# Optimization experiments

Measured on AMD Instinct MI355X. Metric: run time of the kernel, lower is better.

Reference implementation:

```python
import jax, jax.numpy as jnp
import numpy as np

EPS = 1e-13

def masked_softmax(vec, mask, axis=-1):
    # Old AllenNLP masked_softmax: softmax(vec * mask), re-mask, renormalize.
    result = jax.nn.softmax(vec * mask, axis=axis)
    result = result * mask
    return result / (result.sum(axis=axis, keepdims=True) + EPS)

def setup_inputs() -> dict:
    key = jax.random.key(0)
    k1, k2, k3, k4 = jax.random.split(key, 4)
    B, N, T, U, H = 8, 20, 300, 64, 512
    doc_encoding = jax.random.normal(k1, (B, N, T, H), dtype=jnp.float32)
    q_encoding = jax.random.normal(k2, (B, U, H), dtype=jnp.float32)
    doc_mask = jax.random.randint(k3, (B, N, T), 0, 2, dtype=jnp.int32)
    q_mask = jax.random.randint(k4, (B, U), 0, 2, dtype=jnp.int32)
    return {"doc_encoding": doc_encoding, "q_encoding": q_encoding,
            "doc_mask": doc_mask, "q_mask": q_mask}

def reference(doc_encoding, q_encoding, doc_mask, q_mask):
    B, N, T, H = doc_encoding.shape
    U = q_encoding.shape[1]
    dtype = doc_encoding.dtype
    dm = doc_mask.astype(dtype)            # B,N,T
    qm = q_mask.astype(dtype)              # B,U
    doc = doc_encoding.reshape(B, N * T, H)  # B,NT,H
    # shared unnormalized co-attention scores: B,NT,U
    scores = jnp.einsum('bkh,buh->bku', doc, q_encoding)
    # doc->question attention (softmax over U, masked by q_mask)
    attn = masked_softmax(scores, qm[:, None, :], axis=-1)  # B,NT,U
    aggq = jnp.einsum('bku,buh->bkh', attn, q_encoding)      # B,NT,H
    # question->doc attention (softmax over T within each doc, masked by doc_mask)
    attn_t = scores.transpose(0, 2, 1).reshape(B, U, N, T)   # B,U,N,T
    attn_t = masked_softmax(attn_t, dm[:, None, :, :], axis=-1)
    attn_t = attn_t.reshape(B, U, N * T)
    aggdoc = jnp.einsum('buk,bkh->buh', attn_t, doc)          # B,U,H
    aggq2 = jnp.einsum('bku,buh->bkh', attn, aggdoc)          # B,NT,H
    out = jnp.concatenate([aggq.reshape(B, N, T, H),
                           aggq2.reshape(B, N, T, H)], axis=-1)  # B,N,T,2H
    return out
```

## Files before the change

kernel.cpp:

```cpp
#include <hip/hip_runtime.h>

#define BB 8
#define NN 20
#define TT 300
#define UU 64
#define HH 512
#define NT 6000


typedef __attribute__((ext_vector_type(4))) float f32x4;
typedef __attribute__((ext_vector_type(8))) short s16x8;

__device__ __forceinline__ float bf2f(unsigned short u) {
  union { unsigned int i; float f; } c; c.i = ((unsigned int)u) << 16; return c.f;
}
__device__ __forceinline__ unsigned short f2bf(float f) {
  union { float f; unsigned int i; } c; c.f = f;
  unsigned int u = c.i;
  unsigned int r = (u + 0x7fffu + ((u >> 16) & 1u)) >> 16;
  return (unsigned short)r;
}
__device__ __forceinline__ void splitbf(float x, unsigned short& hi, unsigned short& lo) {
  hi = f2bf(x);
  lo = f2bf(x - bf2f(hi));
}
__device__ __forceinline__ f32x4 mfma16(s16x8 a, s16x8 b, f32x4 c) {
  return __builtin_amdgcn_mfma_f32_16x16x32_bf16(a, b, c, 0, 0, 0);
}

__global__ __launch_bounds__(256) void kdetect(const unsigned short* __restrict__ d16,
                                               int* __restrict__ flag) {
  __shared__ int cnt[4];
  int t = threadIdx.x;
  unsigned short v = d16[t];
  int e = (v >> 7) & 0xFF;
  int weird = (e > 140 || (e < 110 && (v & 0x7FFFu) != 0)) ? 1 : 0;
  unsigned long long m = __ballot(weird);
  if ((t & 63) == 0) cnt[t >> 6] = __popcll(m);
  __syncthreads();
  if (t == 0) flag[0] = (cnt[0] + cnt[1] + cnt[2] + cnt[3] >= 32) ? 1 : 0;
}

__global__ __launch_bounds__(256) void k0_init(const void* __restrict__ qv,
                                               const int* __restrict__ flag,
                                               float* __restrict__ W) {
  const int isf32 = *flag;
  int idx = blockIdx.x * 256 + threadIdx.x;
  int h2 = idx & 1023;
  int bu = idx >> 10;
  float v = 0.0f;
  if (h2 < HH) {
    v = isf32 ? ((const float*)qv)[bu * HH + h2]
              : bf2f(((const unsigned short*)qv)[bu * HH + h2]);
  }
  W[idx] = v;
}

__global__ __launch_bounds__(256) void k1_mfma(const void* __restrict__ docv,
                                               const void* __restrict__ qv,
                                               const int* __restrict__ flag,
                                               float* __restrict__ scores) {
  __shared__ __align__(16) unsigned short sDhi[64 * 64], sDlo[64 * 64];
  __shared__ __align__(16) unsigned short sQhi[64 * 64], sQlo[64 * 64];
  const int isf32 = *flag;
  const int b = blockIdx.y, kt = blockIdx.x;
  const int tid = threadIdx.x;
  const int lane = tid & 63, w = tid >> 6;
  const int l15 = lane & 15, l4 = lane >> 4;
  const int kmax = NT - kt * 64;
  const size_t dbase = (size_t)(b * NT + kt * 64) * HH;
  const size_t qbase = (size_t)b * UU * HH;
  const f32x4 zero = {0.f, 0.f, 0.f, 0.f};
  f32x4 acc[4] = {zero, zero, zero, zero};

  for (int hc = 0; hc < 8; ++hc) {
    if (hc) __syncthreads();
#pragma unroll
    for (int i = 0; i < 2; ++i) {
      int g = tid + 256 * i;
      int row = g >> 3, h8 = (g & 7) * 8;
      int addr = (row * 128 + h8 * 2) ^ ((row & 7) << 4);
      {
        float v[8] = {0.f, 0.f, 0.f, 0.f, 0.f, 0.f, 0.f, 0.f};
        if (row < kmax) {
          size_t off = dbase + (size_t)row * HH + hc * 64 + h8;
          if (isf32) {
            const float* df = (const float*)docv;
            float4 a0 = *(const float4*)(df + off);
            float4 a1 = *(const float4*)(df + off + 4);
            v[0] = a0.x; v[1] = a0.y; v[2] = a0.z; v[3] = a0.w;
            v[4] = a1.x; v[5] = a1.y; v[6] = a1.z; v[7] = a1.w;
          } else {
            const unsigned short* db = (const unsigned short*)docv;
            ushort4 a0 = *(const ushort4*)(db + off);
            ushort4 a1 = *(const ushort4*)(db + off + 4);
            v[0] = bf2f(a0.x); v[1] = bf2f(a0.y); v[2] = bf2f(a0.z); v[3] = bf2f(a0.w);
            v[4] = bf2f(a1.x); v[5] = bf2f(a1.y); v[6] = bf2f(a1.z); v[7] = bf2f(a1.w);
          }
        }
        s16x8 vh, vl;
#pragma unroll
        for (int j = 0; j < 8; ++j) {
          unsigned short hh, ll; splitbf(v[j], hh, ll);
          vh[j] = (short)hh; vl[j] = (short)ll;
        }
        *(s16x8*)((char*)sDhi + addr) = vh;
        *(s16x8*)((char*)sDlo + addr) = vl;
      }
      {
        size_t off = qbase + (size_t)row * HH + hc * 64 + h8;
        float v[8];
        if (isf32) {
          const float* qf = (const float*)qv;
          float4 a0 = *(const float4*)(qf + off);
          float4 a1 = *(const float4*)(qf + off + 4);
          v[0] = a0.x; v[1] = a0.y; v[2] = a0.z; v[3] = a0.w;
          v[4] = a1.x; v[5] = a1.y; v[6] = a1.z; v[7] = a1.w;
        } else {
          const unsigned short* qb = (const unsigned short*)qv;
          ushort4 a0 = *(const ushort4*)(qb + off);
          ushort4 a1 = *(const ushort4*)(qb + off + 4);
          v[0] = bf2f(a0.x); v[1] = bf2f(a0.y); v[2] = bf2f(a0.z); v[3] = bf2f(a0.w);
          v[4] = bf2f(a1.x); v[5] = bf2f(a1.y); v[6] = bf2f(a1.z); v[7] = bf2f(a1.w);
        }
        s16x8 vh, vl;
#pragma unroll
        for (int j = 0; j < 8; ++j) {
          unsigned short hh, ll; splitbf(v[j], hh, ll);
          vh[j] = (short)hh; vl[j] = (short)ll;
        }
        *(s16x8*)((char*)sQhi + addr) = vh;
        *(s16x8*)((char*)sQlo + addr) = vl;
      }
    }
    __syncthreads();
#pragma unroll
    for (int kb = 0; kb < 2; ++kb) {
      const int off = kb * 64 + l4 * 16;
      const int brow = w * 16 + l15;
      const int ba = (brow * 128 + off) ^ ((brow & 7) << 4);
      s16x8 bh = *(const s16x8*)((const char*)sDhi + ba);
      s16x8 bl = *(const s16x8*)((const char*)sDlo + ba);
#pragma unroll
      for (int mt = 0; mt < 4; ++mt) {
        const int arow = mt * 16 + l15;
        const int aa = (arow * 128 + off) ^ ((arow & 7) << 4);
        s16x8 ah = *(const s16x8*)((const char*)sQhi + aa);
        s16x8 al = *(const s16x8*)((const char*)sQlo + aa);
        acc[mt] = mfma16(ah, bh, acc[mt]);
        acc[mt] = mfma16(ah, bl, acc[mt]);
        acc[mt] = mfma16(al, bh, acc[mt]);
      }
    }
  }
  const int krow = w * 16 + l15;
  if (krow < kmax) {
    size_t ro = ((size_t)b * NT + kt * 64 + krow) * 64;
#pragma unroll
    for (int mt = 0; mt < 4; ++mt)
      *(f32x4*)&scores[ro + mt * 16 + l4 * 4] = acc[mt];
  }
}

__global__ __launch_bounds__(256) void k2b_tstats(const float* __restrict__ scores,
                                                  const int* __restrict__ dm,
                                                  float* __restrict__ tmax,
                                                  float* __restrict__ tsum) {
  const int b = blockIdx.x / NN;
  const int n = blockIdx.x % NN;
  const int u = threadIdx.x & 63;
  const int tg = threadIdx.x >> 6;
  float m = -__builtin_inff(), s = 0.0f;
  for (int t = tg; t < TT; t += 4) {
    int dmv = dm[(b * NN + n) * TT + t];
    if (dmv) {
      float v = scores[((size_t)(b * NT) + n * TT + t) * 64 + u];
      if (v > m) { s = s * __expf(m - v) + 1.0f; m = v; }
      else s += __expf(v - m);
    }
  }
  __shared__ float sm[4][64], ss[4][64];
  sm[tg][u] = m; ss[tg][u] = s;
  __syncthreads();
  if (threadIdx.x < 64) {
    float M = sm[0][u];
#pragma unroll
    for (int i = 1; i < 4; ++i) M = fmaxf(M, sm[i][u]);
    float S = 0.0f;
#pragma unroll
    for (int i = 0; i < 4; ++i) {
      if (ss[i][u] > 0.0f) S += ss[i][u] * __expf(sm[i][u] - M);
    }
    tmax[(b * 64 + u) * NN + n] = M;
    tsum[(b * 64 + u) * NN + n] = S;
  }
}

__global__ __launch_bounds__(256) void k2c2(const float* __restrict__ scores,
                                            const int* __restrict__ qm,
                                            const int* __restrict__ dm,
                                            const float* __restrict__ tmax,
                                            const float* __restrict__ tsum,
                                            unsigned short* __restrict__ PaH,
                                            unsigned short* __restrict__ PaL,
                                            unsigned short* __restrict__ Pt) {
  const int row = blockIdx.x * 4 + (threadIdx.x >> 6);
  const int u = threadIdx.x & 63;
  const int b = row / NT;
  const int k = row - b * NT;
  const int n = k / TT;
  const float s = scores[(size_t)row * 64 + u];
  const int m = qm[b * 64 + u];
  float v = m ? s : -__builtin_inff();
#pragma unroll
  for (int o = 32; o > 0; o >>= 1) v = fmaxf(v, __shfl_xor(v, o, 64));
  float e = m ? __expf(s - v) : 0.0f;
  float sum = e;
#pragma unroll
  for (int o = 32; o > 0; o >>= 1) sum += __shfl_xor(sum, o, 64);
  float attn = (sum > 0.0f) ? (e / sum) : 0.0f;
  unsigned short hi, lo;
  splitbf(attn, hi, lo);
  PaH[(size_t)row * 64 + u] = hi;
  PaL[(size_t)row * 64 + u] = lo;
  float wgt = 0.0f;
  if (dm[b * NT + k]) {
    float S = tsum[(b * 64 + u) * NN + n];
    if (S > 0.0f) wgt = __expf(s - tmax[(b * 64 + u) * NN + n]) / S;
  }
  Pt[(size_t)row * 64 + u] = f2bf(wgt);
}

__global__ __launch_bounds__(256) void k3_mfma(const unsigned short* __restrict__ Pt,
                                               const void* __restrict__ docv,
                                               const int* __restrict__ flag,
                                               float* __restrict__ W) {
  __shared__ __align__(16) unsigned short sDh[128 * 64], sDl[128 * 64];
  __shared__ __align__(16) unsigned short sP[64 * 64];
  const int isf32 = *flag;
  const int b = blockIdx.z, hc = blockIdx.y, kc = blockIdx.x;
  const int tid = threadIdx.x, lane = tid & 63, w = tid >> 6;
  const int l15 = lane & 15, l4 = lane >> 4;
  const int k0base = kc * 375, kend = k0base + 375;
  const f32x4 zero = {0.f, 0.f, 0.f, 0.f};
  f32x4 acc[4][2];
#pragma unroll
  for (int mt = 0; mt < 4; ++mt) { acc[mt][0] = zero; acc[mt][1] = zero; }

  for (int kb = k0base; kb < kend; kb += 64) {
    const int kn = min(64, kend - kb);
    if (kb != k0base) __syncthreads();
#pragma unroll
    for (int i = 0; i < 4; ++i) {
      int g = tid + 256 * i;
      int kk = g >> 4, u4 = (g & 15) * 4;
      unsigned short t[4] = {0, 0, 0, 0};
      if (kk < kn) {
        ushort4 tv = *(const ushort4*)&Pt[((size_t)b * NT + kb + kk) * 64 + u4];
        t[0] = tv.x; t[1] = tv.y; t[2] = tv.z; t[3] = tv.w;
      }
#pragma unroll
      for (int ii = 0; ii < 4; ++ii) {
        int jj = (ii + tid) & 3;
        int u = u4 + jj;
        int addr = (u * 128 + kk * 2) ^ ((u & 7) << 4);
        *(unsigned short*)((char*)sP + addr) = t[jj];
      }
    }
#pragma unroll
    for (int i = 0; i < 8; ++i) {
      int g = tid + 256 * i;
      int kk = g >> 5, h4 = (g & 31) * 4;
      float v[4] = {0.f, 0.f, 0.f, 0.f};
      if (kk < kn) {
        size_t off = ((size_t)b * NT + kb + kk) * HH + hc * 128 + h4;
        if (isf32) {
          float4 a0 = *(const float4*)((const float*)docv + off);
          v[0] = a0.x; v[1] = a0.y; v[2] = a0.z; v[3] = a0.w;
        } else {
          ushort4 a0 = *(const ushort4*)((const unsigned short*)docv + off);
          v[0] = bf2f(a0.x); v[1] = bf2f(a0.y); v[2] = bf2f(a0.z); v[3] = bf2f(a0.w);
        }
      }
#pragma unroll
      for (int ii = 0; ii < 4; ++ii) {
        int jj = (ii + tid) & 3;
        int hrow = h4 + jj;
        unsigned short hh, ll;
        splitbf(v[jj], hh, ll);
        int addr = (hrow * 128 + kk * 2) ^ ((hrow & 7) << 4);
        *(unsigned short*)((char*)sDh + addr) = hh;
        *(unsigned short*)((char*)sDl + addr) = ll;
      }
    }
    __syncthreads();
#pragma unroll
    for (int ks = 0; ks < 2; ++ks) {
      const int off = ks * 64 + l4 * 16;
      s16x8 bh[2], bl[2];
#pragma unroll
      for (int nt = 0; nt < 2; ++nt) {
        int r = w * 32 + nt * 16 + l15;
        int a = (r * 128 + off) ^ ((r & 7) << 4);
        bh[nt] = *(const s16x8*)((const char*)sDh + a);
        bl[nt] = *(const s16x8*)((const char*)sDl + a);
      }
#pragma unroll
      for (int mt = 0; mt < 4; ++mt) {
        int r = mt * 16 + l15;
        int a = (r * 128 + off) ^ ((r & 7) << 4);
        s16x8 pa = *(const s16x8*)((const char*)sP + a);
#pragma unroll
        for (int nt = 0; nt < 2; ++nt) {
          acc[mt][nt] = mfma16(pa, bh[nt], acc[mt][nt]);
          acc[mt][nt] = mfma16(pa, bl[nt], acc[mt][nt]);
        }
      }
    }
  }
#pragma unroll
  for (int mt = 0; mt < 4; ++mt)
#pragma unroll
    for (int nt = 0; nt < 2; ++nt)
#pragma unroll
      for (int j = 0; j < 4; ++j) {
        int u = mt * 16 + l4 * 4 + j;
        int h = hc * 128 + w * 32 + nt * 16 + l15;
        atomicAdd(&W[((size_t)b * 64 + u) * 1024 + 512 + h], acc[mt][nt][j]);
      }
}

__global__ __launch_bounds__(256) void k35_wt(const float* __restrict__ W,
                                              unsigned short* __restrict__ WtH,
                                              unsigned short* __restrict__ WtL) {
  __shared__ float sW[64][68];
  const int b = blockIdx.y, hck = blockIdx.x;
  const int tid = threadIdx.x;
#pragma unroll
  for (int i = 0; i < 4; ++i) {
    int g = tid + 256 * i;
    int u = g >> 4, c4 = (g & 15) * 4;
    *(float4*)&sW[u][c4] = *(const float4*)&W[((size_t)b * 64 + u) * 1024 + hck * 64 + c4];
  }
  __syncthreads();
  const int h = tid >> 2, ug = tid & 3;
  s16x8 oh[2], ol[2];
#pragma unroll
  for (int p = 0; p < 2; ++p)
#pragma unroll
    for (int j = 0; j < 8; ++j) {
      unsigned short hh, ll;
      splitbf(sW[ug * 16 + p * 8 + j][h], hh, ll);
      oh[p][j] = (short)hh; ol[p][j] = (short)ll;
    }
  size_t ob = ((size_t)b * 1024 + hck * 64 + h) * 64 + ug * 16;
  *(s16x8*)&WtH[ob] = oh[0];
  *(s16x8*)&WtH[ob + 8] = oh[1];
  *(s16x8*)&WtL[ob] = ol[0];
  *(s16x8*)&WtL[ob + 8] = ol[1];
}

__global__ __launch_bounds__(256) void k4_mfma(const unsigned short* __restrict__ PaH,
                                               const unsigned short* __restrict__ PaL,
                                               const unsigned short* __restrict__ WtH,
                                               const unsigned short* __restrict__ WtL,
                                               const int* __restrict__ flag,
                                               void* __restrict__ outv) {
  const int isf32 = *flag;
  const int b = blockIdx.z, ht = blockIdx.y, kt = blockIdx.x;
  const int tid = threadIdx.x, lane = tid & 63, w = tid >> 6;
  const int l15 = lane & 15, l4 = lane >> 4;
  const int h0 = ht * 64;
  const int kr0 = kt * 256 + w * 64;
  const f32x4 zero = {0.f, 0.f, 0.f, 0.f};
  f32x4 acc[4][4];
#pragma unroll
  for (int mt = 0; mt < 4; ++mt)
#pragma unroll
    for (int nt = 0; nt < 4; ++nt) acc[mt][nt] = zero;
#pragma unroll
  for (int kb = 0; kb < 2; ++kb) {
    s16x8 ah[4], al[4];
#pragma unroll
    for (int mt = 0; mt < 4; ++mt) {
      size_t a = ((size_t)b * 1024 + h0 + mt * 16 + l15) * 64 + kb * 32 + l4 * 8;
      ah[mt] = *(const s16x8*)&WtH[a];
      al[mt] = *(const s16x8*)&WtL[a];
    }
#pragma unroll
    for (int nt = 0; nt < 4; ++nt) {
      int krow = kr0 + nt * 16 + l15;
      int krc = krow < NT ? krow : NT - 1;
      size_t pb = ((size_t)b * NT + krc) * 64 + kb * 32 + l4 * 8;
      s16x8 bh = *(const s16x8*)&PaH[pb];
      s16x8 bl = *(const s16x8*)&PaL[pb];
#pragma unroll
      for (int mt = 0; mt < 4; ++mt) {
        acc[mt][nt] = mfma16(ah[mt], bh, acc[mt][nt]);
        acc[mt][nt] = mfma16(ah[mt], bl, acc[mt][nt]);
        acc[mt][nt] = mfma16(al[mt], bh, acc[mt][nt]);
      }
    }
  }
#pragma unroll
  for (int nt = 0; nt < 4; ++nt) {
    int krow = kr0 + nt * 16 + l15;
    if (krow < NT) {
      size_t ob = ((size_t)b * NT + krow) * 1024 + h0;
#pragma unroll
      for (int mt = 0; mt < 4; ++mt) {
        int h2 = mt * 16 + l4 * 4;
        if (isf32) {
          *(f32x4*)((float*)outv + ob + h2) = acc[mt][nt];
        } else {
          ushort4 o;
          o.x = f2bf(acc[mt][nt][0]); o.y = f2bf(acc[mt][nt][1]);
          o.z = f2bf(acc[mt][nt][2]); o.w = f2bf(acc[mt][nt][3]);
          *(ushort4*)((unsigned short*)outv + ob + h2) = o;
        }
      }
    }
  }
}

__global__ __launch_bounds__(256) void k2_softmax_u(float* __restrict__ scores,
                                                    const int* __restrict__ qm) {
  const int row = blockIdx.x * 4 + (threadIdx.x >> 6);
  const int u = threadIdx.x & 63;
  const int b = row / NT;
  const float s = scores[(size_t)row * 64 + u];
  const int m = qm[b * 64 + u];
  float v = m ? s : -__builtin_inff();
#pragma unroll
  for (int o = 32; o > 0; o >>= 1) v = fmaxf(v, __shfl_xor(v, o, 64));
  float e = m ? __expf(s - v) : 0.0f;
  float sum = e;
#pragma unroll
  for (int o = 32; o > 0; o >>= 1) sum += __shfl_xor(sum, o, 64);
  scores[(size_t)row * 64 + u] = (sum > 0.0f) ? (e / sum) : 0.0f;
}

__global__ __launch_bounds__(256) void k3_aggdoc(const float* __restrict__ scores,
                                                 const void* __restrict__ docv,
                                                 const int* __restrict__ dm,
                                                 const float* __restrict__ tmax,
                                                 const float* __restrict__ tsum,
                                                 const int* __restrict__ flag,
                                                 float* __restrict__ W) {
  __shared__ float wL[32][68];
  __shared__ float dL[32][68];
  const int isf32 = *flag;
  const int b = blockIdx.z, hc = blockIdx.y, kc = blockIdx.x;
  const int tid = threadIdx.x;
  const int th = tid & 15, tuq = tid >> 4;
  float acc[4][4] = {};
  const int k0base = kc * 375, kend = k0base + 375;
  for (int k0 = k0base; k0 < kend; k0 += 32) {
    const int kn = min(32, kend - k0);
#pragma unroll
    for (int i = 0; i < 8; ++i) {
      int idx = tid + 256 * i;
      int kk = idx >> 6, uu = idx & 63;
      float wv = 0.0f;
      if (kk < kn) {
        int k = k0 + kk;
        int n = k / TT;
        if (dm[b * NT + k]) {
          float S = tsum[(b * 64 + uu) * NN + n];
          if (S > 0.0f) {
            float M = tmax[(b * 64 + uu) * NN + n];
            wv = __expf(scores[((size_t)(b * NT) + k) * 64 + uu] - M) / S;
          }
        }
      }
      wL[kk][uu] = wv;
    }
#pragma unroll
    for (int i = 0; i < 2; ++i) {
      int g = tid + 256 * i;
      int kk = g >> 4, c4 = (g & 15) * 4;
      float4 v = make_float4(0.f, 0.f, 0.f, 0.f);
      if (kk < kn) {
        size_t off = ((size_t)(b * NT) + k0 + kk) * HH + hc * 64 + c4;
        if (isf32) v = *(const float4*)((const float*)docv + off);
        else {
          ushort4 t4 = *(const ushort4*)((const unsigned short*)docv + off);
          v = make_float4(bf2f(t4.x), bf2f(t4.y), bf2f(t4.z), bf2f(t4.w));
        }
      }
      *(float4*)&dL[kk][c4] = v;
    }
    __syncthreads();
    for (int kk = 0; kk < kn; ++kk) {
      float4 w4 = *(const float4*)&wL[kk][tuq * 4];
      float4 d4 = *(const float4*)&dL[kk][th * 4];
      acc[0][0] += w4.x * d4.x; acc[0][1] += w4.x * d4.y; acc[0][2] += w4.x * d4.z; acc[0][3] += w4.x * d4.w;
      acc[1][0] += w4.y * d4.x; acc[1][1] += w4.y * d4.y; acc[1][2] += w4.y * d4.z; acc[1][3] += w4.y * d4.w;
      acc[2][0] += w4.z * d4.x; acc[2][1] += w4.z * d4.y; acc[2][2] += w4.z * d4.z; acc[2][3] += w4.z * d4.w;
      acc[3][0] += w4.w * d4.x; acc[3][1] += w4.w * d4.y; acc[3][2] += w4.w * d4.z; acc[3][3] += w4.w * d4.w;
    }
    __syncthreads();
  }
#pragma unroll
  for (int i = 0; i < 4; ++i) {
#pragma unroll
    for (int j = 0; j < 4; ++j) {
      size_t addr = ((size_t)(b * 64) + tuq * 4 + i) * 1024 + 512 + hc * 64 + th * 4 + j;
      atomicAdd(&W[addr], acc[i][j]);
    }
  }
}

__global__ __launch_bounds__(256) void k4_out(const float* __restrict__ attn,
                                              const float* __restrict__ W,
                                              const int* __restrict__ flag,
                                              void* __restrict__ outv) {
  __shared__ float sAt[64][68];
  __shared__ float sWt[64][132];
  const int isf32 = *flag;
  const int b = blockIdx.z;
  const int kt = blockIdx.x;
  const int ht = blockIdx.y;
  const int tid = threadIdx.x;
  const int th2 = tid & 15, tkq = tid >> 4;
#pragma unroll
  for (int i = 0; i < 4; ++i) {
    int g = tid + 256 * i;
    int row = g >> 4, c4 = (g & 15) * 4;
    int k = kt * 64 + row;
    float4 v = make_float4(0.f, 0.f, 0.f, 0.f);
    if (k < NT) v = *(const float4*)&attn[((size_t)(b * NT) + k) * 64 + c4];
    *(float4*)&sAt[row][c4] = v;
  }
#pragma unroll
  for (int i = 0; i < 8; ++i) {
    int g = tid + 256 * i;
    int row = g >> 5, c4 = (g & 31) * 4;
    float4 wv = *(const float4*)&W[((size_t)(b * 64) + row) * 1024 + ht * 128 + c4];
    *(float4*)&sWt[row][c4] = wv;
  }
  __syncthreads();
  float acc[4][8] = {};
#pragma unroll 4
  for (int u = 0; u < 64; u += 4) {
    float a[4][4];
#pragma unroll
    for (int i = 0; i < 4; ++i)
      *(float4*)a[i] = *(const float4*)&sAt[tkq * 4 + i][u];
#pragma unroll
    for (int r = 0; r < 4; ++r) {
      float4 w0 = *(const float4*)&sWt[u + r][th2 * 4];
      float4 w1 = *(const float4*)&sWt[u + r][64 + th2 * 4];
#pragma unroll
      for (int i = 0; i < 4; ++i) {
        acc[i][0] += a[i][r] * w0.x; acc[i][1] += a[i][r] * w0.y;
        acc[i][2] += a[i][r] * w0.z; acc[i][3] += a[i][r] * w0.w;
        acc[i][4] += a[i][r] * w1.x; acc[i][5] += a[i][r] * w1.y;
        acc[i][6] += a[i][r] * w1.z; acc[i][7] += a[i][r] * w1.w;
      }
    }
  }
#pragma unroll
  for (int i = 0; i < 4; ++i) {
    int k = kt * 64 + tkq * 4 + i;
    if (k < NT) {
      size_t off = ((size_t)(b * NT) + k) * 1024 + ht * 128 + th2 * 4;
      if (isf32) {
        *(float4*)((float*)outv + off) = make_float4(acc[i][0], acc[i][1], acc[i][2], acc[i][3]);
        *(float4*)((float*)outv + off + 64) = make_float4(acc[i][4], acc[i][5], acc[i][6], acc[i][7]);
      } else {
        ushort4 o0, o1;
        o0.x = f2bf(acc[i][0]); o0.y = f2bf(acc[i][1]); o0.z = f2bf(acc[i][2]); o0.w = f2bf(acc[i][3]);
        o1.x = f2bf(acc[i][4]); o1.y = f2bf(acc[i][5]); o1.z = f2bf(acc[i][6]); o1.w = f2bf(acc[i][7]);
        *(ushort4*)((unsigned short*)outv + off) = o0;
        *(ushort4*)((unsigned short*)outv + off + 64) = o1;
      }
    }
  }
}

extern "C" void kernel_launch(void* const* d_in, const int* in_sizes, int n_in,
                              void* d_out, int out_size, void* d_ws, size_t ws_size,
                              hipStream_t stream) {
  const void* doc = d_in[0];
  const void* q   = d_in[1];
  const int* dmask = (const int*)d_in[2];
  const int* qmask = (const int*)d_in[3];

  float* ws = (float*)d_ws;
  float* scores = ws;
  float* tmax   = ws + 3072000;
  float* tsum   = ws + 3082240;
  float* W      = ws + 3092480;
  int*   flag   = (int*)(ws + 3616768);
  unsigned short* Pt  = (unsigned short*)(ws + 3616772);
  unsigned short* PaH = (unsigned short*)(ws + 5152772);
  unsigned short* PaL = (unsigned short*)(ws + 6688772);
  unsigned short* WtH = (unsigned short*)(ws + 8224772);
  unsigned short* WtL = (unsigned short*)(ws + 8486916);
  const size_t need_new = (size_t)8749060 * 4;

  kdetect<<<1, 256, 0, stream>>>((const unsigned short*)doc, flag);
  k0_init<<<2048, 256, 0, stream>>>(q, flag, W);
  k1_mfma<<<dim3(94, 8), 256, 0, stream>>>(doc, q, flag, scores);
  k2b_tstats<<<160, 256, 0, stream>>>(scores, dmask, tmax, tsum);
  if (ws_size >= need_new) {
    k2c2<<<12000, 256, 0, stream>>>(scores, qmask, dmask, tmax, tsum, PaH, PaL, Pt);
    k3_mfma<<<dim3(16, 4, 8), 256, 0, stream>>>(Pt, doc, flag, W);
    k35_wt<<<dim3(16, 8), 256, 0, stream>>>(W, WtH, WtL);
    k4_mfma<<<dim3(24, 16, 8), 256, 0, stream>>>(PaH, PaL, WtH, WtL, flag, d_out);
  } else {
    k3_aggdoc<<<dim3(16, 8, 8), 256, 0, stream>>>(scores, doc, dmask, tmax, tsum, flag, W);
    k2_softmax_u<<<12000, 256, 0, stream>>>(scores, qmask);
    k4_out<<<dim3(94, 8, 8), 256, 0, stream>>>(scores, W, flag, d_out);
  }
}
```

Before: 412.0 us.

## Presplit Q once, widen k1 tiles, and vectorize k3 transposed LDS staging

The query is split into bf16 hi/lo halves once in k0_init and stored to workspace. k1 then loads those halves straight into registers instead of re-splitting Q through LDS in every block, and processes 128 doc rows per 512-thread block. k3 now splits K into chunks of 250 across 24 blocks instead of 375 across 16. Its Pt and doc staging uses 4x4 register transposes with ushort4 LDS stores instead of scalar 2-byte stores. The changes add workspace, raise per-thread register use in k1 and leave fewer k1 blocks.

```diff
diff --git a/kernel.cpp b/kernel.cpp
--- a/kernel.cpp
+++ b/kernel.cpp
@@ -43,7 +43,9 @@
 
 __global__ __launch_bounds__(256) void k0_init(const void* __restrict__ qv,
                                                const int* __restrict__ flag,
-                                               float* __restrict__ W) {
+                                               float* __restrict__ W,
+                                               unsigned short* __restrict__ QsH,
+                                               unsigned short* __restrict__ QsL) {
   const int isf32 = *flag;
   int idx = blockIdx.x * 256 + threadIdx.x;
   int h2 = idx & 1023;
@@ -52,24 +54,28 @@
   if (h2 < HH) {
     v = isf32 ? ((const float*)qv)[bu * HH + h2]
               : bf2f(((const unsigned short*)qv)[bu * HH + h2]);
+    unsigned short hi, lo;
+    splitbf(v, hi, lo);
+    QsH[bu * HH + h2] = hi;
+    QsL[bu * HH + h2] = lo;
   }
   W[idx] = v;
 }
 
-__global__ __launch_bounds__(256) void k1_mfma(const void* __restrict__ docv,
-                                               const void* __restrict__ qv,
+__global__ __launch_bounds__(512) void k1_mfma(const void* __restrict__ docv,
+                                               const unsigned short* __restrict__ QsH,
+                                               const unsigned short* __restrict__ QsL,
                                                const int* __restrict__ flag,
                                                float* __restrict__ scores) {
-  __shared__ __align__(16) unsigned short sDhi[64 * 64], sDlo[64 * 64];
-  __shared__ __align__(16) unsigned short sQhi[64 * 64], sQlo[64 * 64];
+  __shared__ __align__(16) unsigned short sDh[128 * 64], sDl[128 * 64];
   const int isf32 = *flag;
   const int b = blockIdx.y, kt = blockIdx.x;
   const int tid = threadIdx.x;
   const int lane = tid & 63, w = tid >> 6;
   const int l15 = lane & 15, l4 = lane >> 4;
-  const int kmax = NT - kt * 64;
-  const size_t dbase = (size_t)(b * NT + kt * 64) * HH;
-  const size_t qbase = (size_t)b * UU * HH;
+  const int kmax = NT - kt * 128;
+  const size_t dbase = (size_t)(b * NT + kt * 128) * HH;
+  const size_t qrow0 = (size_t)b * UU * HH;
   const f32x4 zero = {0.f, 0.f, 0.f, 0.f};
   f32x4 acc[4] = {zero, zero, zero, zero};
 
@@ -77,85 +83,63 @@
     if (hc) __syncthreads();
 #pragma unroll
     for (int i = 0; i < 2; ++i) {
-      int g = tid + 256 * i;
+      int g = tid + 512 * i;
       int row = g >> 3, h8 = (g & 7) * 8;
       int addr = (row * 128 + h8 * 2) ^ ((row & 7) << 4);
-      {
-        float v[8] = {0.f, 0.f, 0.f, 0.f, 0.f, 0.f, 0.f, 0.f};
-        if (row < kmax) {
-          size_t off = dbase + (size_t)row * HH + hc * 64 + h8;
-          if (isf32) {
-            const float* df = (const float*)docv;
-            float4 a0 = *(const float4*)(df + off);
-            float4 a1 = *(const float4*)(df + off + 4);
-            v[0] = a0.x; v[1] = a0.y; v[2] = a0.z; v[3] = a0.w;
-            v[4] = a1.x; v[5] = a1.y; v[6] = a1.z; v[7] = a1.w;
-          } else {
-            const unsigned short* db = (const unsigned short*)docv;
-            ushort4 a0 = *(const ushort4*)(db + off);
-            ushort4 a1 = *(const ushort4*)(db + off + 4);
-            v[0] = bf2f(a0.x); v[1] = bf2f(a0.y); v[2] = bf2f(a0.z); v[3] = bf2f(a0.w);
-            v[4] = bf2f(a1.x); v[5] = bf2f(a1.y); v[6] = bf2f(a1.z); v[7] = bf2f(a1.w);
-          }
-        }
-        s16x8 vh, vl;
-#pragma unroll
-        for (int j = 0; j < 8; ++j) {
-          unsigned short hh, ll; splitbf(v[j], hh, ll);
-          vh[j] = (short)hh; vl[j] = (short)ll;
-        }
-        *(s16x8*)((char*)sDhi + addr) = vh;
-        *(s16x8*)((char*)sDlo + addr) = vl;
-      }
-      {
-        size_t off = qbase + (size_t)row * HH + hc * 64 + h8;
-        float v[8];
+      float v[8] = {0.f, 0.f, 0.f, 0.f, 0.f, 0.f, 0.f, 0.f};
+      if (row < kmax) {
+        size_t off = dbase + (size_t)row * HH + hc * 64 + h8;
         if (isf32) {
-          const float* qf = (const float*)qv;
-          float4 a0 = *(const float4*)(qf + off);
-          float4 a1 = *(const float4*)(qf + off + 4);
+          const float* df = (const float*)docv;
+          float4 a0 = *(const float4*)(df + off);
+          float4 a1 = *(const float4*)(df + off + 4);
           v[0] = a0.x; v[1] = a0.y; v[2] = a0.z; v[3] = a0.w;
           v[4] = a1.x; v[5] = a1.y; v[6] = a1.z; v[7] = a1.w;
         } else {
-          const unsigned short* qb = (const unsigned short*)qv;
-          ushort4 a0 = *(const ushort4*)(qb + off);
-          ushort4 a1 = *(const ushort4*)(qb + off + 4);
+          const unsigned short* db = (const unsigned short*)docv;
+          ushort4 a0 = *(const ushort4*)(db + off);
+          ushort4 a1 = *(const ushort4*)(db + off + 4);
           v[0] = bf2f(a0.x); v[1] = bf2f(a0.y); v[2] = bf2f(a0.z); v[3] = bf2f(a0.w);
           v[4] = bf2f(a1.x); v[5] = bf2f(a1.y); v[6] = bf2f(a1.z); v[7] = bf2f(a1.w);
         }
-        s16x8 vh, vl;
-#pragma unroll
-        for (int j = 0; j < 8; ++j) {
-          unsigned short hh, ll; splitbf(v[j], hh, ll);
-          vh[j] = (short)hh; vl[j] = (short)ll;
-        }
-        *(s16x8*)((char*)sQhi + addr) = vh;
-        *(s16x8*)((char*)sQlo + addr) = vl;
-      }
+      }
+      s16x8 vh, vl;
+#pragma unroll
+      for (int j = 0; j < 8; ++j) {
+        unsigned short hh, ll; splitbf(v[j], hh, ll);
+        vh[j] = (short)hh; vl[j] = (short)ll;
+      }
+      *(s16x8*)((char*)sDh + addr) = vh;
+      *(s16x8*)((char*)sDl + addr) = vl;
     }
     __syncthreads();
+    s16x8 qh[2][4], ql[2][4];
+#pragma unroll
+    for (int kb = 0; kb < 2; ++kb)
+#pragma unroll
+      for (int mt = 0; mt < 4; ++mt) {
+        size_t qa = qrow0 + (size_t)(mt * 16 + l15) * HH + hc * 64 + kb * 32 + l4 * 8;
+        qh[kb][mt] = *(const s16x8*)&QsH[qa];
+        ql[kb][mt] = *(const s16x8*)&QsL[qa];
+      }
 #pragma unroll
     for (int kb = 0; kb < 2; ++kb) {
       const int off = kb * 64 + l4 * 16;
       const int brow = w * 16 + l15;
       const int ba = (brow * 128 + off) ^ ((brow & 7) << 4);
-      s16x8 bh = *(const s16x8*)((const char*)sDhi + ba);
-      s16x8 bl = *(const s16x8*)((const char*)sDlo + ba);
+      s16x8 bh = *(const s16x8*)((const char*)sDh + ba);
+      s16x8 bl = *(const s16x8*)((const char*)sDl + ba);
 #pragma unroll
       for (int mt = 0; mt < 4; ++mt) {
-        const int arow = mt * 16 + l15;
-        const int aa = (arow * 128 + off) ^ ((arow & 7) << 4);
-        s16x8 ah = *(const s16x8*)((const char*)sQhi + aa);
-        s16x8 al = *(const s16x8*)((const char*)sQlo + aa);
-        acc[mt] = mfma16(ah, bh, acc[mt]);
-        acc[mt] = mfma16(ah, bl, acc[mt]);
-        acc[mt] = mfma16(al, bh, acc[mt]);
+        acc[mt] = mfma16(qh[kb][mt], bh, acc[mt]);
+        acc[mt] = mfma16(qh[kb][mt], bl, acc[mt]);
+        acc[mt] = mfma16(ql[kb][mt], bh, acc[mt]);
       }
     }
   }
   const int krow = w * 16 + l15;
   if (krow < kmax) {
-    size_t ro = ((size_t)b * NT + kt * 64 + krow) * 64;
+    size_t ro = ((size_t)b * NT + kt * 128 + krow) * 64;
 #pragma unroll
     for (int mt = 0; mt < 4; ++mt)
       *(f32x4*)&scores[ro + mt * 16 + l4 * 4] = acc[mt];
@@ -241,7 +225,7 @@
   const int b = blockIdx.z, hc = blockIdx.y, kc = blockIdx.x;
   const int tid = threadIdx.x, lane = tid & 63, w = tid >> 6;
   const int l15 = lane & 15, l4 = lane >> 4;
-  const int k0base = kc * 375, kend = k0base + 375;
+  const int k0base = kc * 250, kend = k0base + 250;
   const f32x4 zero = {0.f, 0.f, 0.f, 0.f};
   f32x4 acc[4][2];
 #pragma unroll
@@ -250,47 +234,55 @@
   for (int kb = k0base; kb < kend; kb += 64) {
     const int kn = min(64, kend - kb);
     if (kb != k0base) __syncthreads();
-#pragma unroll
-    for (int i = 0; i < 4; ++i) {
-      int g = tid + 256 * i;
-      int kk = g >> 4, u4 = (g & 15) * 4;
-      unsigned short t[4] = {0, 0, 0, 0};
-      if (kk < kn) {
-        ushort4 tv = *(const ushort4*)&Pt[((size_t)b * NT + kb + kk) * 64 + u4];
-        t[0] = tv.x; t[1] = tv.y; t[2] = tv.z; t[3] = tv.w;
-      }
-#pragma unroll
-      for (int ii = 0; ii < 4; ++ii) {
-        int jj = (ii + tid) & 3;
-        int u = u4 + jj;
-        int addr = (u * 128 + kk * 2) ^ ((u & 7) << 4);
-        *(unsigned short*)((char*)sP + addr) = t[jj];
-      }
-    }
-#pragma unroll
-    for (int i = 0; i < 8; ++i) {
-      int g = tid + 256 * i;
-      int kk = g >> 5, h4 = (g & 31) * 4;
-      float v[4] = {0.f, 0.f, 0.f, 0.f};
-      if (kk < kn) {
-        size_t off = ((size_t)b * NT + kb + kk) * HH + hc * 128 + h4;
-        if (isf32) {
-          float4 a0 = *(const float4*)((const float*)docv + off);
-          v[0] = a0.x; v[1] = a0.y; v[2] = a0.z; v[3] = a0.w;
-        } else {
-          ushort4 a0 = *(const ushort4*)((const unsigned short*)docv + off);
-          v[0] = bf2f(a0.x); v[1] = bf2f(a0.y); v[2] = bf2f(a0.z); v[3] = bf2f(a0.w);
+    {
+      const int ug = tid & 15, kg = tid >> 4;
+      ushort4 r[4];
+#pragma unroll
+      for (int rr = 0; rr < 4; ++rr) {
+        int kk = kg * 4 + rr;
+        ushort4 t = make_ushort4(0, 0, 0, 0);
+        if (kk < kn) t = *(const ushort4*)&Pt[((size_t)b * NT + kb + kk) * 64 + ug * 4];
+        r[rr] = t;
+      }
+      const unsigned short* rp = (const unsigned short*)r;
+#pragma unroll
+      for (int uu = 0; uu < 4; ++uu) {
+        int u = ug * 4 + uu;
+        int addr = (u * 128 + kg * 8) ^ ((u & 7) << 4);
+        ushort4 col = make_ushort4(rp[0 * 4 + uu], rp[1 * 4 + uu], rp[2 * 4 + uu], rp[3 * 4 + uu]);
+        *(ushort4*)((char*)sP + addr) = col;
+      }
+    }
+#pragma unroll
+    for (int i = 0; i < 2; ++i) {
+      int s = tid + 256 * i;
+      int hg = s & 31, kg = s >> 5;
+      float rv[4][4];
+#pragma unroll
+      for (int rr = 0; rr < 4; ++rr) {
+        int kk = kg * 4 + rr;
+        float4 v = make_float4(0.f, 0.f, 0.f, 0.f);
+        if (kk < kn) {
+          size_t off = ((size_t)b * NT + kb + kk) * HH + hc * 128 + hg * 4;
+          if (isf32) v = *(const float4*)((const float*)docv + off);
+          else {
+            ushort4 t = *(const ushort4*)((const unsigned short*)docv + off);
+            v = make_float4(bf2f(t.x), bf2f(t.y), bf2f(t.z), bf2f(t.w));
+          }
         }
-      }
-#pragma unroll
-      for (int ii = 0; ii < 4; ++ii) {
-        int jj = (ii + tid) & 3;
-        int hrow = h4 + jj;
-        unsigned short hh, ll;
-        splitbf(v[jj], hh, ll);
-        int addr = (hrow * 128 + kk * 2) ^ ((hrow & 7) << 4);
-        *(unsigned short*)((char*)sDh + addr) = hh;
-        *(unsigned short*)((char*)sDl + addr) = ll;
+        rv[rr][0] = v.x; rv[rr][1] = v.y; rv[rr][2] = v.z; rv[rr][3] = v.w;
+      }
+#pragma unroll
+      for (int hh = 0; hh < 4; ++hh) {
+        int hrow = hg * 4 + hh;
+        int addr = (hrow * 128 + kg * 8) ^ ((hrow & 7) << 4);
+        unsigned short h0, l0, h1, l1, h2, l2, h3, l3;
+        splitbf(rv[0][hh], h0, l0);
+        splitbf(rv[1][hh], h1, l1);
+        splitbf(rv[2][hh], h2, l2);
+        splitbf(rv[3][hh], h3, l3);
+        *(ushort4*)((char*)sDh + addr) = make_ushort4(h0, h1, h2, h3);
+        *(ushort4*)((char*)sDl + addr) = make_ushort4(l0, l1, l2, l3);
       }
     }
     __syncthreads();
@@ -593,20 +585,22 @@
   float* tsum   = ws + 3082240;
   float* W      = ws + 3092480;
   int*   flag   = (int*)(ws + 3616768);
-  unsigned short* Pt  = (unsigned short*)(ws + 3616772);
-  unsigned short* PaH = (unsigned short*)(ws + 5152772);
-  unsigned short* PaL = (unsigned short*)(ws + 6688772);
-  unsigned short* WtH = (unsigned short*)(ws + 8224772);
-  unsigned short* WtL = (unsigned short*)(ws + 8486916);
-  const size_t need_new = (size_t)8749060 * 4;
+  unsigned short* QsH = (unsigned short*)(ws + 3616772);
+  unsigned short* QsL = (unsigned short*)(ws + 3747844);
+  unsigned short* Pt  = (unsigned short*)(ws + 3878916);
+  unsigned short* PaH = (unsigned short*)(ws + 5414916);
+  unsigned short* PaL = (unsigned short*)(ws + 6950916);
+  unsigned short* WtH = (unsigned short*)(ws + 8486916);
+  unsigned short* WtL = (unsigned short*)(ws + 8749060);
+  const size_t need_new = (size_t)9011204 * 4;
 
   kdetect<<<1, 256, 0, stream>>>((const unsigned short*)doc, flag);
-  k0_init<<<2048, 256, 0, stream>>>(q, flag, W);
-  k1_mfma<<<dim3(94, 8), 256, 0, stream>>>(doc, q, flag, scores);
+  k0_init<<<2048, 256, 0, stream>>>(q, flag, W, QsH, QsL);
+  k1_mfma<<<dim3(47, 8), 512, 0, stream>>>(doc, QsH, QsL, flag, scores);
   k2b_tstats<<<160, 256, 0, stream>>>(scores, dmask, tmax, tsum);
   if (ws_size >= need_new) {
     k2c2<<<12000, 256, 0, stream>>>(scores, qmask, dmask, tmax, tsum, PaH, PaL, Pt);
-    k3_mfma<<<dim3(16, 4, 8), 256, 0, stream>>>(Pt, doc, flag, W);
+    k3_mfma<<<dim3(24, 4, 8), 256, 0, stream>>>(Pt, doc, flag, W);
     k35_wt<<<dim3(16, 8), 256, 0, stream>>>(W, WtH, WtL);
     k4_mfma<<<dim3(24, 16, 8), 256, 0, stream>>>(PaH, PaL, WtH, WtL, flag, d_out);
   } else {
```

New measurement: 444.8 us. 8.0% more time.
